# Performance work log

Measured on AMD Instinct MI355X. Metric: run time of the kernel, lower is better.

Reference implementation:

```python
import jax, jax.numpy as jnp
import numpy as np

NUM_GRAPHS = 32

def leaky(x):
    return jax.nn.leaky_relu(x, 0.1)

def setup_inputs() -> dict:
    key = jax.random.key(0)
    ks = jax.random.split(key, 32)
    N, E = 8000, 32000
    x = jax.random.normal(ks[0], (N, 4), dtype=jnp.float32)
    edge_index = jax.random.randint(ks[1], (2, E), 0, N, dtype=jnp.int32)
    batch_index = jnp.sort(jax.random.randint(ks[2], (N,), 0, NUM_GRAPHS, dtype=jnp.int32))
    def lin(k, i, o, s=0.1):
        k1, k2 = jax.random.split(k)
        return jax.random.normal(k1, (i, o), dtype=jnp.float32) * s, jax.random.normal(k2, (o,), dtype=jnp.float32) * s
    p = {}
    # edge networks: Linear(3,64)+LeakyReLU+Linear(64, in*out)+LeakyReLU
    p['en1_w1'], p['en1_b1'] = lin(ks[3], 3, 64)
    p['en1_w2'], p['en1_b2'] = lin(ks[4], 64, 4 * 8)
    p['en2_w1'], p['en2_b1'] = lin(ks[5], 3, 64)
    p['en2_w2'], p['en2_b2'] = lin(ks[6], 64, 8 * 64)
    p['en3_w1'], p['en3_b1'] = lin(ks[7], 3, 64)
    p['en3_w2'], p['en3_b2'] = lin(ks[8], 64, 64 * 128)
    # NNConv root weights + biases
    p['root1'], p['cb1'] = lin(ks[9], 4, 8)
    p['root2'], p['cb2'] = lin(ks[10], 8, 64)
    p['root3'], p['cb3'] = lin(ks[11], 64, 128)
    # readout MLP
    p['fc1_w'], p['fc1_b'] = lin(ks[12], 128, 128)
    p['fc2_w'], p['fc2_b'] = lin(ks[13], 128, 64)
    p['fc3_w'], p['fc3_b'] = lin(ks[14], 64, 1)
    return dict(x=x, edge_index=edge_index, batch_index=batch_index, **p)

def nnconv(h, edge_index, edge_attr, w1, b1, w2, b2, root, cbias, in_ch, out_ch):
    # per-edge weight matrix from edge attributes
    e = leaky(edge_attr @ w1 + b1)              # [E,64]
    W = leaky(e @ w2 + b2).reshape(-1, in_ch, out_ch)  # [E,in,out]
    msg = jnp.einsum('ei,eio->eo', h[edge_index[0]], W)  # gather + per-edge matmul
    agg = jax.ops.segment_sum(msg, edge_index[1], num_segments=h.shape[0])  # scatter-add
    return agg + h @ root + cbias

def reference(x, edge_index, batch_index, en1_w1, en1_b1, en1_w2, en1_b2, en2_w1, en2_b1, en2_w2, en2_b2, en3_w1, en3_b1, en3_w2, en3_b2, root1, cb1, root2, cb2, root3, cb3, fc1_w, fc1_b, fc2_w, fc2_b, fc3_w, fc3_b):
    edge_attr = (x[edge_index[1]] - x[edge_index[0]])[:, 1:]  # [E,3] relative position
    h = leaky(nnconv(x, edge_index, edge_attr, en1_w1, en1_b1, en1_w2, en1_b2, root1, cb1, 4, 8))
    h = leaky(nnconv(h, edge_index, edge_attr, en2_w1, en2_b1, en2_w2, en2_b2, root2, cb2, 8, 64))
    h = leaky(nnconv(h, edge_index, edge_attr, en3_w1, en3_b1, en3_w2, en3_b2, root3, cb3, 64, 128))
    g = jax.ops.segment_sum(h, batch_index, num_segments=NUM_GRAPHS)  # sum-pool per graph
    g = leaky(g @ fc1_w + fc1_b)
    g = leaky(g @ fc2_w + fc2_b)
    return g @ fc3_w + fc3_b  # [G,1] total energies
```

## Files before the change

kernel.cpp:

```cpp
#include <hip/hip_runtime.h>
#include <hip/hip_bf16.h>

typedef __attribute__((ext_vector_type(8))) short short8;
typedef __attribute__((ext_vector_type(4))) float floatx4;

__device__ __forceinline__ float leaky(float v){ return v > 0.f ? v : 0.1f*v; }
__device__ __forceinline__ void atomAdd(float* p, float v){ unsafeAtomicAdd(p, v); }
__device__ __forceinline__ short f2bf(float f){
  __hip_bfloat16 h = __float2bfloat16(f);
  return *reinterpret_cast<short*>(&h);
}

__global__ void efeat_all(const float* __restrict__ x, const int* __restrict__ ei,
                          const float* __restrict__ w1a, const float* __restrict__ b1a,
                          const float* __restrict__ w1b, const float* __restrict__ b1b,
                          const float* __restrict__ w1c, const float* __restrict__ b1c,
                          float* __restrict__ ef1, short* __restrict__ ef2b,
                          short* __restrict__ ef3b, int E, int Epad){
  int id = blockIdx.x*256 + threadIdx.x;
  if (id >= Epad*64) return;
  int e = id >> 6, j = id & 63;
  if (e >= E){ ef1[id] = 0.f; ef2b[id] = 0; ef3b[id] = 0; return; }
  int s = ei[e], d = ei[E+e];
  float a0 = x[d*4+1] - x[s*4+1];
  float a1 = x[d*4+2] - x[s*4+2];
  float a2 = x[d*4+3] - x[s*4+3];
  float v1 = leaky(a0*w1a[j] + a1*w1a[64+j] + a2*w1a[128+j] + b1a[j]);
  float v2 = leaky(a0*w1b[j] + a1*w1b[64+j] + a2*w1b[128+j] + b1b[j]);
  float v3 = leaky(a0*w1c[j] + a1*w1c[64+j] + a2*w1c[128+j] + b1c[j]);
  ef1[id] = v1;
  ef2b[id] = f2bf(v2);
  ef3b[id] = f2bf(v3);
}

template<int IC, int OC>
__global__ void pack_w2(const float* __restrict__ w2, short* __restrict__ w2p){
  constexpr int OT = OC/16;
  int tid = blockIdx.x*256 + threadIdx.x;
  int lane = tid & 63;
  int c = tid >> 6;
  if (c >= IC*OT*2) return;
  int kh = c & 1;
  int rem = c >> 1;
  int otg = rem % OT;
  int i = rem / OT;
  int n = lane & 15, q = lane >> 4;
  short out[8];
  #pragma unroll
  for (int j=0;j<8;j++){
    int k = kh*32 + q*8 + j;
    out[j] = f2bf(w2[(size_t)k*(IC*OC) + i*OC + otg*16 + n]);
  }
  *reinterpret_cast<short8*>(w2p + (size_t)c*512 + lane*8) = *reinterpret_cast<short8*>(out);
}

__global__ void conv1_kernel(const float* __restrict__ ef, const float* __restrict__ x,
                             const int* __restrict__ ei, const float* __restrict__ w2,
                             const float* __restrict__ b2, float* __restrict__ agg, int E){
  int id = blockIdx.x*256 + threadIdx.x;
  if (id >= E*8) return;
  int e = id >> 3, o = id & 7;
  int s = ei[e], d = ei[E+e];
  const float* efe = ef + (size_t)e*64;
  float z[4];
  #pragma unroll
  for (int i=0;i<4;i++) z[i] = b2[i*8+o];
  for (int k=0;k<64;k++){
    float a = efe[k];
    #pragma unroll
    for (int i=0;i<4;i++) z[i] += a*w2[k*32 + i*8 + o];
  }
  float msg = 0.f;
  #pragma unroll
  for (int i=0;i<4;i++) msg += x[s*4+i]*leaky(z[i]);
  atomAdd(&agg[d*8+o], msg);
}

template<int IC, int OC>
__global__ void node_kernel(float* __restrict__ h, const float* __restrict__ hin,
                            const float* __restrict__ root, const float* __restrict__ cb, int N){
  int id = blockIdx.x*256 + threadIdx.x;
  if (id >= N*OC) return;
  int n = id / OC, o = id % OC;
  float v = h[id] + cb[o];
  const float* hi = hin + (size_t)n*IC;
  #pragma unroll
  for (int i=0;i<IC;i++) v += hi[i]*root[i*OC+o];
  h[id] = leaky(v);
}

template<int IC, int OC>
__global__ __launch_bounds__(256)
void conv_mfma(const short* __restrict__ efb, const float* __restrict__ h,
               const int* __restrict__ ei, const short* __restrict__ w2p,
               const float* __restrict__ b2, float* __restrict__ agg,
               int E, int Epad){
  constexpr int OT  = OC/16;
  constexpr int WOT = OT/4;
  __shared__ float hsT[IC][64];
  __shared__ int sdst[64];
  int tid = threadIdx.x;
  int eb = blockIdx.x*64;

  {
    int e = tid & 63;
    int ge = eb + e;
    bool valid = ge < E;
    int src = valid ? ei[ge] : 0;
    if constexpr (IC == 64){
      int i0 = (tid >> 6) * 16;
      const float4* hp = reinterpret_cast<const float4*>(h + (size_t)src*64 + i0);
      #pragma unroll
      for (int r=0;r<4;r++){
        float4 hv = valid ? hp[r] : float4{0.f,0.f,0.f,0.f};
        hsT[i0 + r*4 + 0][e] = hv.x;
        hsT[i0 + r*4 + 1][e] = hv.y;
        hsT[i0 + r*4 + 2][e] = hv.z;
        hsT[i0 + r*4 + 3][e] = hv.w;
      }
    } else {
      int i0 = (tid >> 6) * 2;
      float2 hv = valid ? *reinterpret_cast<const float2*>(h + (size_t)src*8 + i0)
                        : float2{0.f,0.f};
      hsT[i0 + 0][e] = hv.x;
      hsT[i0 + 1][e] = hv.y;
    }
    if (tid < 64) sdst[tid] = (eb + tid < E) ? ei[E + eb + tid] : -1;
  }
  __syncthreads();

  int lane = tid & 63;
  int wv = tid >> 6;
  int n = lane & 15, quad = lane >> 4;
  int o0 = wv * (OC/4);

  short8 A[4][2];
  #pragma unroll
  for (int m=0;m<4;m++)
    #pragma unroll
    for (int kh=0;kh<2;kh++)
      A[m][kh] = *reinterpret_cast<const short8*>(efb + (size_t)(eb + m*16 + n)*64 + kh*32 + quad*8);

  float msg[4][WOT][4];
  #pragma unroll
  for (int m=0;m<4;m++)
    #pragma unroll
    for (int t=0;t<WOT;t++)
      #pragma unroll
      for (int r=0;r<4;r++) msg[m][t][r] = 0.f;

  for (int i=0;i<IC;i++){
    short8 B[WOT][2];
    float bz[WOT];
    #pragma unroll
    for (int t=0;t<WOT;t++){
      int otg = (o0 >> 4) + t;
      #pragma unroll
      for (int kh=0;kh<2;kh++)
        B[t][kh] = *reinterpret_cast<const short8*>(w2p + ((size_t)((i*OT + otg)*2 + kh) << 9) + lane*8);
      bz[t] = b2[i*OC + o0 + t*16 + n];
    }
    #pragma unroll
    for (int m=0;m<4;m++){
      float4 hv = *reinterpret_cast<const float4*>(&hsT[i][m*16 + quad*4]);
      #pragma unroll
      for (int t=0;t<WOT;t++){
        floatx4 z = {bz[t], bz[t], bz[t], bz[t]};
        z = __builtin_amdgcn_mfma_f32_16x16x32_bf16(A[m][0], B[t][0], z, 0, 0, 0);
        z = __builtin_amdgcn_mfma_f32_16x16x32_bf16(A[m][1], B[t][1], z, 0, 0, 0);
        float l0 = fmaxf(z[0], 0.1f*z[0]);
        float l1 = fmaxf(z[1], 0.1f*z[1]);
        float l2 = fmaxf(z[2], 0.1f*z[2]);
        float l3 = fmaxf(z[3], 0.1f*z[3]);
        msg[m][t][0] += hv.x*l0;
        msg[m][t][1] += hv.y*l1;
        msg[m][t][2] += hv.z*l2;
        msg[m][t][3] += hv.w*l3;
      }
    }
  }

  #pragma unroll
  for (int m=0;m<4;m++){
    #pragma unroll
    for (int r=0;r<4;r++){
      int d = sdst[m*16 + quad*4 + r];
      if (d >= 0){
        #pragma unroll
        for (int t=0;t<WOT;t++)
          atomAdd(&agg[(size_t)d*OC + o0 + t*16 + n], msg[m][t][r]);
      }
    }
  }
}

__global__ void pool_kernel(const float* __restrict__ h3, const int* __restrict__ batch,
                            float* __restrict__ g, int N){
  int o = threadIdx.x;
  int n0 = blockIdx.x*64;
  if (n0 >= N) return;
  float acc = 0.f;
  int cur = batch[n0];
  for (int r=0;r<64;r++){
    int n = n0 + r;
    if (n >= N) break;
    int b = batch[n];
    if (b != cur){ atomAdd(&g[cur*128+o], acc); acc = 0.f; cur = b; }
    acc += h3[(size_t)n*128+o];
  }
  atomAdd(&g[cur*128+o], acc);
}

__global__ void head_kernel(const float* __restrict__ g,
                            const float* __restrict__ fc1w, const float* __restrict__ fc1b,
                            const float* __restrict__ fc2w, const float* __restrict__ fc2b,
                            const float* __restrict__ fc3w, const float* __restrict__ fc3b,
                            float* __restrict__ out){
  __shared__ float s1[128], s2[128];
  int gi = blockIdx.x, t = threadIdx.x;
  s1[t] = g[gi*128+t];
  __syncthreads();
  float v = fc1b[t];
  for (int i=0;i<128;i++) v += s1[i]*fc1w[i*128+t];
  s2[t] = leaky(v);
  __syncthreads();
  if (t < 64){
    float v2 = fc2b[t];
    for (int i=0;i<128;i++) v2 += s2[i]*fc2w[i*64+t];
    s1[t] = leaky(v2);
  }
  __syncthreads();
  if (t == 0){
    float v3 = fc3b[0];
    for (int i=0;i<64;i++) v3 += s1[i]*fc3w[i];
    out[gi] = v3;
  }
}

extern "C" void kernel_launch(void* const* d_in, const int* in_sizes, int n_in,
                              void* d_out, int out_size, void* d_ws, size_t ws_size,
                              hipStream_t stream) {
  const float* x      = (const float*)d_in[0];
  const int*   ei     = (const int*)  d_in[1];
  const int*   batch  = (const int*)  d_in[2];
  const float* en1_w1 = (const float*)d_in[3];  const float* en1_b1 = (const float*)d_in[4];
  const float* en1_w2 = (const float*)d_in[5];  const float* en1_b2 = (const float*)d_in[6];
  const float* en2_w1 = (const float*)d_in[7];  const float* en2_b1 = (const float*)d_in[8];
  const float* en2_w2 = (const float*)d_in[9];  const float* en2_b2 = (const float*)d_in[10];
  const float* en3_w1 = (const float*)d_in[11]; const float* en3_b1 = (const float*)d_in[12];
  const float* en3_w2 = (const float*)d_in[13]; const float* en3_b2 = (const float*)d_in[14];
  const float* root1  = (const float*)d_in[15]; const float* cb1    = (const float*)d_in[16];
  const float* root2  = (const float*)d_in[17]; const float* cb2    = (const float*)d_in[18];
  const float* root3  = (const float*)d_in[19]; const float* cb3    = (const float*)d_in[20];
  const float* fc1w   = (const float*)d_in[21]; const float* fc1b   = (const float*)d_in[22];
  const float* fc2w   = (const float*)d_in[23]; const float* fc2b   = (const float*)d_in[24];
  const float* fc3w   = (const float*)d_in[25]; const float* fc3b   = (const float*)d_in[26];
  float* out = (float*)d_out;

  const int N = in_sizes[0] / 4;
  const int E = in_sizes[1] / 2;
  const int G = 32;
  const int Epad = (E + 63) & ~63;

  float* ef1  = (float*)d_ws;
  short* ef2b = (short*)(ef1 + (size_t)Epad*64);
  short* ef3b = ef2b + (size_t)Epad*64;
  short* w2p2 = ef3b + (size_t)Epad*64;
  short* w2p3 = w2p2 + 8*4*2*512;
  float* a1   = (float*)(w2p3 + 64*8*2*512);
  float* a2   = a1 + (size_t)N*8;
  float* a3   = a2 + (size_t)N*64;
  float* g    = a3 + (size_t)N*128;

  size_t zero_bytes = ((size_t)N*(8+64+128) + (size_t)G*128) * sizeof(float);
  hipMemsetAsync(a1, 0, zero_bytes, stream);

  efeat_all<<<(Epad*64 + 255)/256, 256, 0, stream>>>(
      x, ei, en1_w1, en1_b1, en2_w1, en2_b1, en3_w1, en3_b1,
      ef1, ef2b, ef3b, E, Epad);

  pack_w2<8,64><<<(8*4*2*64 + 255)/256, 256, 0, stream>>>(en2_w2, w2p2);
  pack_w2<64,128><<<(64*8*2*64 + 255)/256, 256, 0, stream>>>(en3_w2, w2p3);

  conv1_kernel<<<(E*8 + 255)/256, 256, 0, stream>>>(ef1, x, ei, en1_w2, en1_b2, a1, E);
  node_kernel<4,8><<<(N*8 + 255)/256, 256, 0, stream>>>(a1, x, root1, cb1, N);

  conv_mfma<8,64><<<Epad/64, 256, 0, stream>>>(ef2b, a1, ei, w2p2, en2_b2, a2, E, Epad);
  node_kernel<8,64><<<(N*64 + 255)/256, 256, 0, stream>>>(a2, a1, root2, cb2, N);

  conv_mfma<64,128><<<Epad/64, 256, 0, stream>>>(ef3b, a2, ei, w2p3, en3_b2, a3, E, Epad);
  node_kernel<64,128><<<(N*128 + 255)/256, 256, 0, stream>>>(a3, a2, root3, cb3, N);

  pool_kernel<<<(N + 63)/64, 128, 0, stream>>>(a3, batch, g, N);
  head_kernel<<<G, 128, 0, stream>>>(g, fc1w, fc1b, fc2w, fc2b, fc3w, fc3b, out);
}
```

Baseline: 261.4 us.

## Split conv3 over input channels, shrink conv2 tiles, fuse node3 with pooling

The MFMA edge-conv kernel is templated on edge-tile size and input-channel split. Conv2 now uses 32-edge blocks, and conv3 splits its 64 input channels across two blocks, giving more blocks in flight and possibly better occupancy. The price is more atomics into the aggregation buffer and reloading the A fragments in each split. The two pack_w2 launches merge into one, and the layer-3 node update is fused with graph sum-pooling via per-element atomics, removing a kernel and an intermediate pass.

```diff
diff --git a/kernel.cpp b/kernel.cpp
--- a/kernel.cpp
+++ b/kernel.cpp
@@ -33,17 +33,16 @@
   ef3b[id] = f2bf(v3);
 }
 
-template<int IC, int OC>
-__global__ void pack_w2(const float* __restrict__ w2, short* __restrict__ w2p){
-  constexpr int OT = OC/16;
-  int tid = blockIdx.x*256 + threadIdx.x;
-  int lane = tid & 63;
-  int c = tid >> 6;
-  if (c >= IC*OT*2) return;
-  int kh = c & 1;
-  int rem = c >> 1;
-  int otg = rem % OT;
-  int i = rem / OT;
+__global__ void pack_w2_all(const float* __restrict__ w2a, short* __restrict__ pa,
+                            const float* __restrict__ w2b, short* __restrict__ pb){
+  int bid = blockIdx.x;
+  const float* w2; short* dst; int IC, OC, cbase;
+  if (bid < 16){ w2 = w2a; dst = pa; IC = 8;  OC = 64;  cbase = bid*4; }
+  else        { w2 = w2b; dst = pb; IC = 64; OC = 128; cbase = (bid-16)*4; }
+  int lane = threadIdx.x & 63;
+  int c = cbase + (threadIdx.x >> 6);
+  int OT = OC/16;
+  int kh = c & 1; int rem = c >> 1; int otg = rem % OT; int i = rem / OT;
   int n = lane & 15, q = lane >> 4;
   short out[8];
   #pragma unroll
@@ -51,7 +50,7 @@
     int k = kh*32 + q*8 + j;
     out[j] = f2bf(w2[(size_t)k*(IC*OC) + i*OC + otg*16 + n]);
   }
-  *reinterpret_cast<short8*>(w2p + (size_t)c*512 + lane*8) = *reinterpret_cast<short8*>(out);
+  *reinterpret_cast<short8*>(dst + (size_t)c*512 + lane*8) = *reinterpret_cast<short8*>(out);
 }
 
 __global__ void conv1_kernel(const float* __restrict__ ef, const float* __restrict__ x,
@@ -89,43 +88,60 @@
   h[id] = leaky(v);
 }
 
-template<int IC, int OC>
+__global__ void node3_pool(const float* __restrict__ agg, const float* __restrict__ hin,
+                           const float* __restrict__ root, const float* __restrict__ cb,
+                           const int* __restrict__ batch, float* __restrict__ g, int N){
+  int id = blockIdx.x*256 + threadIdx.x;
+  if (id >= N*128) return;
+  int n = id >> 7, o = id & 127;
+  float v = agg[id] + cb[o];
+  const float* hi = hin + (size_t)n*64;
+  #pragma unroll
+  for (int i=0;i<64;i++) v += hi[i]*root[i*128+o];
+  atomAdd(&g[batch[n]*128 + o], leaky(v));
+}
+
+template<int IC, int OC, int MB, int ICB>
 __global__ __launch_bounds__(256)
 void conv_mfma(const short* __restrict__ efb, const float* __restrict__ h,
                const int* __restrict__ ei, const short* __restrict__ w2p,
-               const float* __restrict__ b2, float* __restrict__ agg,
-               int E, int Epad){
-  constexpr int OT  = OC/16;
-  constexpr int WOT = OT/4;
-  __shared__ float hsT[IC][64];
-  __shared__ int sdst[64];
+               const float* __restrict__ b2, float* __restrict__ agg, int E){
+  constexpr int ME   = MB*16;
+  constexpr int OT   = OC/16;
+  constexpr int WOT  = OT/4;
+  constexpr int NSPL = IC/ICB;
+  __shared__ float hsT[ICB][ME];
+  __shared__ int sdst[ME];
   int tid = threadIdx.x;
-  int eb = blockIdx.x*64;
+  int bi = blockIdx.x;
+  int eb = (bi / NSPL) * ME;
+  int i0 = (bi % NSPL) * ICB;
 
   {
-    int e = tid & 63;
+    int e = tid % ME;
     int ge = eb + e;
     bool valid = ge < E;
     int src = valid ? ei[ge] : 0;
-    if constexpr (IC == 64){
-      int i0 = (tid >> 6) * 16;
-      const float4* hp = reinterpret_cast<const float4*>(h + (size_t)src*64 + i0);
-      #pragma unroll
-      for (int r=0;r<4;r++){
-        float4 hv = valid ? hp[r] : float4{0.f,0.f,0.f,0.f};
-        hsT[i0 + r*4 + 0][e] = hv.x;
-        hsT[i0 + r*4 + 1][e] = hv.y;
-        hsT[i0 + r*4 + 2][e] = hv.z;
-        hsT[i0 + r*4 + 3][e] = hv.w;
+    constexpr int CH  = 256/ME;
+    constexpr int IPC = ICB/CH;
+    int c = tid / ME;
+    const float* hp = h + (size_t)src*IC + i0 + c*IPC;
+    if constexpr (IPC == 8){
+      #pragma unroll
+      for (int half=0; half<2; half++){
+        float4 hv = valid ? reinterpret_cast<const float4*>(hp)[half]
+                          : float4{0.f,0.f,0.f,0.f};
+        hsT[c*IPC + half*4 + 0][e] = hv.x;
+        hsT[c*IPC + half*4 + 1][e] = hv.y;
+        hsT[c*IPC + half*4 + 2][e] = hv.z;
+        hsT[c*IPC + half*4 + 3][e] = hv.w;
       }
     } else {
-      int i0 = (tid >> 6) * 2;
-      float2 hv = valid ? *reinterpret_cast<const float2*>(h + (size_t)src*8 + i0)
-                        : float2{0.f,0.f};
-      hsT[i0 + 0][e] = hv.x;
-      hsT[i0 + 1][e] = hv.y;
-    }
-    if (tid < 64) sdst[tid] = (eb + tid < E) ? ei[E + eb + tid] : -1;
+      #pragma unroll
+      for (int j=0;j<IPC;j++)
+        hsT[c*IPC + j][e] = valid ? hp[j] : 0.f;
+    }
+    if (tid < ME) sdst[tid] = (eb + tid < E) ? ei[E + eb + tid] : -1;
   }
   __syncthreads();
 
@@ -134,22 +150,23 @@
   int n = lane & 15, quad = lane >> 4;
   int o0 = wv * (OC/4);
 
-  short8 A[4][2];
-  #pragma unroll
-  for (int m=0;m<4;m++)
+  short8 A[MB][2];
+  #pragma unroll
+  for (int m=0;m<MB;m++)
     #pragma unroll
     for (int kh=0;kh<2;kh++)
       A[m][kh] = *reinterpret_cast<const short8*>(efb + (size_t)(eb + m*16 + n)*64 + kh*32 + quad*8);
 
-  float msg[4][WOT][4];
-  #pragma unroll
-  for (int m=0;m<4;m++)
+  float msg[MB][WOT][4];
+  #pragma unroll
+  for (int m=0;m<MB;m++)
     #pragma unroll
     for (int t=0;t<WOT;t++)
       #pragma unroll
       for (int r=0;r<4;r++) msg[m][t][r] = 0.f;
 
-  for (int i=0;i<IC;i++){
+  for (int i=0;i<ICB;i++){
+    int ig = i0 + i;
     short8 B[WOT][2];
     float bz[WOT];
     #pragma unroll
@@ -157,11 +174,11 @@
       int otg = (o0 >> 4) + t;
       #pragma unroll
       for (int kh=0;kh<2;kh++)
-        B[t][kh] = *reinterpret_cast<const short8*>(w2p + ((size_t)((i*OT + otg)*2 + kh) << 9) + lane*8);
-      bz[t] = b2[i*OC + o0 + t*16 + n];
-    }
-    #pragma unroll
-    for (int m=0;m<4;m++){
+        B[t][kh] = *reinterpret_cast<const short8*>(w2p + ((size_t)((ig*OT + otg)*2 + kh) << 9) + lane*8);
+      bz[t] = b2[ig*OC + o0 + t*16 + n];
+    }
+    #pragma unroll
+    for (int m=0;m<MB;m++){
       float4 hv = *reinterpret_cast<const float4*>(&hsT[i][m*16 + quad*4]);
       #pragma unroll
       for (int t=0;t<WOT;t++){
@@ -181,7 +198,7 @@
   }
 
   #pragma unroll
-  for (int m=0;m<4;m++){
+  for (int m=0;m<MB;m++){
     #pragma unroll
     for (int r=0;r<4;r++){
       int d = sdst[m*16 + quad*4 + r];
@@ -192,23 +209,6 @@
       }
     }
   }
-}
-
-__global__ void pool_kernel(const float* __restrict__ h3, const int* __restrict__ batch,
-                            float* __restrict__ g, int N){
-  int o = threadIdx.x;
-  int n0 = blockIdx.x*64;
-  if (n0 >= N) return;
-  float acc = 0.f;
-  int cur = batch[n0];
-  for (int r=0;r<64;r++){
-    int n = n0 + r;
-    if (n >= N) break;
-    int b = batch[n];
-    if (b != cur){ atomAdd(&g[cur*128+o], acc); acc = 0.f; cur = b; }
-    acc += h3[(size_t)n*128+o];
-  }
-  atomAdd(&g[cur*128+o], acc);
 }
 
 __global__ void head_kernel(const float* __restrict__ g,
@@ -279,18 +279,16 @@
       x, ei, en1_w1, en1_b1, en2_w1, en2_b1, en3_w1, en3_b1,
       ef1, ef2b, ef3b, E, Epad);
 
-  pack_w2<8,64><<<(8*4*2*64 + 255)/256, 256, 0, stream>>>(en2_w2, w2p2);
-  pack_w2<64,128><<<(64*8*2*64 + 255)/256, 256, 0, stream>>>(en3_w2, w2p3);
+  pack_w2_all<<<272, 256, 0, stream>>>(en2_w2, w2p2, en3_w2, w2p3);
 
   conv1_kernel<<<(E*8 + 255)/256, 256, 0, stream>>>(ef1, x, ei, en1_w2, en1_b2, a1, E);
   node_kernel<4,8><<<(N*8 + 255)/256, 256, 0, stream>>>(a1, x, root1, cb1, N);
 
-  conv_mfma<8,64><<<Epad/64, 256, 0, stream>>>(ef2b, a1, ei, w2p2, en2_b2, a2, E, Epad);
+  conv_mfma<8,64,2,8><<<Epad/32, 256, 0, stream>>>(ef2b, a1, ei, w2p2, en2_b2, a2, E);
   node_kernel<8,64><<<(N*64 + 255)/256, 256, 0, stream>>>(a2, a1, root2, cb2, N);
 
-  conv_mfma<64,128><<<Epad/64, 256, 0, stream>>>(ef3b, a2, ei, w2p3, en3_b2, a3, E, Epad);
-  node_kernel<64,128><<<(N*128 + 255)/256, 256, 0, stream>>>(a3, a2, root3, cb3, N);
-
-  pool_kernel<<<(N + 63)/64, 128, 0, stream>>>(a3, batch, g, N);
+  conv_mfma<64,128,4,32><<<(Epad/64)*2, 256, 0, stream>>>(ef3b, a2, ei, w2p3, en3_b2, a3, E);
+  node3_pool<<<(N*128 + 255)/256, 256, 0, stream>>>(a3, a2, root3, cb3, batch, g, N);
+
   head_kernel<<<G, 128, 0, stream>>>(g, fc1w, fc1b, fc2w, fc2b, fc3w, fc3b, out);
 }
```

Result: faster. 254.1 us (-2.8%).
